# Kernel optimization log

Measured on AMD Instinct MI355X. Metric: run time of the kernel, lower is better.

The kernel has to match this reference:

```python
import jax, jax.numpy as jnp
import numpy as np

DT = 0.02
B = 524288
HID = 128


def setup_inputs() -> dict:
    key = jax.random.key(0)
    ks = jax.random.split(key, 11)
    def lin_init(k, fan_in, fan_out):
        # torch nn.Linear default: U(-1/sqrt(fan_in), 1/sqrt(fan_in))
        bound = 1.0 / np.sqrt(fan_in)
        kw, kb = jax.random.split(k)
        W = jax.random.uniform(kw, (fan_in, fan_out), jnp.float32, -bound, bound)
        b = jax.random.uniform(kb, (fan_out,), jnp.float32, -bound, bound)
        return W, b
    W1, b1 = lin_init(ks[0], 2, HID)
    W2, b2 = lin_init(ks[1], HID, HID)
    W3, b3 = lin_init(ks[2], HID, HID)
    W4, b4 = lin_init(ks[3], HID, 1)
    return {
        "q": jax.random.normal(ks[4], (B, 1), jnp.float32),
        "p": jax.random.normal(ks[5], (B, 1), jnp.float32),
        "F_ext": jax.random.normal(ks[6], (B, 1), jnp.float32),
        "W1": W1, "b1": b1, "W2": W2, "b2": b2,
        "W3": W3, "b3": b3, "W4": W4, "b4": b4,
    }


def reference(q, p, F_ext, W1, b1, W2, b2, W3, b3, W4, b4):
    def H_sum(q, p):
        s = jnp.concatenate([q, p], axis=1)          # [B, 2]
        h = jnp.tanh(s @ W1 + b1)                    # [B, 128]
        h = jnp.tanh(h @ W2 + b2)
        h = jnp.tanh(h @ W3 + b3)
        return jnp.sum(h @ W4 + b4)                  # scalar; samples independent
    dH_dq, dH_dp = jax.grad(H_sum, argnums=(0, 1))(q, p)
    dq_dt = dH_dp
    dp_dt = -dH_dq + F_ext
    return jnp.concatenate([dq_dt * DT, dp_dt * DT], axis=1)  # [B, 2]
```

## Files before the change

kernel.cpp:

```cpp
#include <hip/hip_runtime.h>

#define DT 0.02f

typedef __attribute__((ext_vector_type(8))) __bf16 bf16x8;
typedef __attribute__((ext_vector_type(4))) __bf16 bf16x4;
typedef __attribute__((ext_vector_type(4))) float  f32x4;

__device__ __forceinline__ float fast_tanh(float x){
    float e = __builtin_amdgcn_exp2f(x * 2.8853900817779268f);
    return 1.0f - 2.0f * __builtin_amdgcn_rcpf(e + 1.0f);
}
__device__ __forceinline__ char* ldsx(char* base, int m, int j){
    return base + (((m << 8) + (j << 1)) ^ ((m & 7) << 4));
}

template<int MODE>
__device__ __forceinline__ void hnn_gemm(const __bf16* __restrict__ Wg,
                                         char* Xbuf, char* Obuf,
                                         const float* __restrict__ bias,
                                         const float* __restrict__ w4,
                                         const bf16x4 (*m1)[4],
                                         int w, int l)
{
    const int lr = l & 15, lg = l >> 4;
    const int rbase = w * 32;

    f32x4 acc[2][4];
    #pragma unroll
    for (int mt = 0; mt < 2; ++mt)
        #pragma unroll
        for (int nt = 0; nt < 4; ++nt) acc[mt][nt] = 0.0f;

    #pragma unroll
    for (int ks = 0; ks < 4; ++ks){
        const int kb = ks * 32 + lg * 8;
        bf16x8 a[2], b[4];
        #pragma unroll
        for (int mt = 0; mt < 2; ++mt)
            a[mt] = *(const bf16x8*)(Wg + ((rbase + mt * 16 + lr) << 7) + kb);
        #pragma unroll
        for (int nt = 0; nt < 4; ++nt)
            b[nt] = *(const bf16x8*)ldsx(Xbuf, nt * 16 + lr, kb);
        #pragma unroll
        for (int mt = 0; mt < 2; ++mt)
            #pragma unroll
            for (int nt = 0; nt < 4; ++nt)
                acc[mt][nt] = __builtin_amdgcn_mfma_f32_16x16x32_bf16(
                    a[mt], b[nt], acc[mt][nt], 0, 0, 0);
    }

    if (MODE == 1){
        #pragma unroll
        for (int mt = 0; mt < 2; ++mt){
            const int j0 = rbase + mt * 16 + lg * 4;
            const f32x4 bv = *(const f32x4*)(bias + j0);
            #pragma unroll
            for (int nt = 0; nt < 4; ++nt){
                const int m = nt * 16 + lr;
                bf16x4 hv;
                #pragma unroll
                for (int jr = 0; jr < 4; ++jr)
                    hv[jr] = (__bf16)fast_tanh(acc[mt][nt][jr] + bv[jr]);
                *(bf16x4*)ldsx(Obuf, m, j0) = hv;
            }
        }
    } else if (MODE == 4){
        #pragma unroll
        for (int mt = 0; mt < 2; ++mt){
            const int j0 = rbase + mt * 16 + lg * 4;
            const f32x4 bv = *(const f32x4*)(bias + j0);
            const f32x4 wv = *(const f32x4*)(w4 + j0);
            #pragma unroll
            for (int nt = 0; nt < 4; ++nt){
                const int m = nt * 16 + lr;
                bf16x4 gv;
                #pragma unroll
                for (int jr = 0; jr < 4; ++jr){
                    float tt = fast_tanh(acc[mt][nt][jr] + bv[jr]);
                    gv[jr] = (__bf16)(wv[jr] * (1.0f - tt * tt));
                }
                *(bf16x4*)ldsx(Obuf, m, j0) = gv;
            }
        }
    } else if (MODE == 0){
        #pragma unroll
        for (int mt = 0; mt < 2; ++mt){
            const int j0 = rbase + mt * 16 + lg * 4;
            #pragma unroll
            for (int nt = 0; nt < 4; ++nt){
                const int m = nt * 16 + lr;
                bf16x4* hp = (bf16x4*)ldsx(Obuf, m, j0);
                bf16x4 hv = *hp, gv;
                #pragma unroll
                for (int jr = 0; jr < 4; ++jr){
                    float h = (float)hv[jr];
                    gv[jr] = (__bf16)(acc[mt][nt][jr] * (1.0f - h * h));
                }
                *hp = gv;
            }
        }
    } else {
        #pragma unroll
        for (int mt = 0; mt < 2; ++mt){
            const int j0 = rbase + mt * 16 + lg * 4;
            #pragma unroll
            for (int nt = 0; nt < 4; ++nt){
                const int m = nt * 16 + lr;
                const bf16x4 mv = m1[mt][nt];
                bf16x4 gv;
                #pragma unroll
                for (int jr = 0; jr < 4; ++jr)
                    gv[jr] = (__bf16)(acc[mt][nt][jr] * (float)mv[jr]);
                *(bf16x4*)ldsx(Obuf, m, j0) = gv;
            }
        }
    }
}

__global__ void hnn_prep(const float* __restrict__ W2, const float* __restrict__ W3,
                         __bf16* __restrict__ ws)
{
    int idx = blockIdx.x * 256 + threadIdx.x;
    int k = idx >> 7, n = idx & 127;
    __bf16 v2 = (__bf16)W2[idx];
    __bf16 v3 = (__bf16)W3[idx];
    ws[n * 128 + k]         = v2;
    ws[16384 + n * 128 + k] = v3;
    ws[32768 + idx]         = v2;
    ws[49152 + idx]         = v3;
}

__global__ __launch_bounds__(256, 4)
void hnn_main(const float* __restrict__ q, const float* __restrict__ p,
              const float* __restrict__ Fx,
              const float* __restrict__ W1, const float* __restrict__ b1,
              const float* __restrict__ b2, const float* __restrict__ b3,
              const float* __restrict__ W4,
              const __bf16* __restrict__ ws,
              float* __restrict__ out)
{
    __shared__ char bufA[16384];
    __shared__ char bufB[16384];
    const int t = threadIdx.x;
    const int w = t >> 6, l = t & 63;
    const int lr = l & 15, lg = l >> 4;
    const long mg0 = (long)blockIdx.x * 64;

    bf16x4 mask1[2][4];
    {
        const int rbase = w * 32;
        float qq[4], pp[4];
        #pragma unroll
        for (int nt = 0; nt < 4; ++nt){
            qq[nt] = q[mg0 + nt * 16 + lr];
            pp[nt] = p[mg0 + nt * 16 + lr];
        }
        #pragma unroll
        for (int mt = 0; mt < 2; ++mt){
            const int j0 = rbase + mt * 16 + lg * 4;
            const f32x4 wq = *(const f32x4*)(W1 + j0);
            const f32x4 wp = *(const f32x4*)(W1 + 128 + j0);
            const f32x4 bb = *(const f32x4*)(b1 + j0);
            #pragma unroll
            for (int nt = 0; nt < 4; ++nt){
                bf16x4 hv, mv;
                #pragma unroll
                for (int jr = 0; jr < 4; ++jr){
                    float h = fast_tanh(fmaf(qq[nt], wq[jr], fmaf(pp[nt], wp[jr], bb[jr])));
                    hv[jr] = (__bf16)h;
                    mv[jr] = (__bf16)(1.0f - h * h);
                }
                *(bf16x4*)ldsx(bufA, nt * 16 + lr, j0) = hv;
                mask1[mt][nt] = mv;
            }
        }
    }
    __syncthreads();
    hnn_gemm<1>(ws,         bufA, bufB, b2, nullptr, nullptr, w, l);
    __syncthreads();
    hnn_gemm<4>(ws + 16384, bufB, bufA, b3, W4, nullptr, w, l);
    __syncthreads();
    hnn_gemm<0>(ws + 49152, bufA, bufB, nullptr, nullptr, nullptr, w, l);
    __syncthreads();
    hnn_gemm<5>(ws + 32768, bufB, bufA, nullptr, nullptr, mask1, w, l);
    __syncthreads();

    {
        const int m = t & 63, q4 = t >> 6;
        float sdq = 0.f, sdp = 0.f;
        #pragma unroll
        for (int i = 0; i < 4; ++i){
            int j0 = q4 * 32 + i * 8;
            bf16x8 gv = *(const bf16x8*)ldsx(bufA, m, j0);
            f32x4 wq0 = *(const f32x4*)(W1 + j0),       wq1 = *(const f32x4*)(W1 + j0 + 4);
            f32x4 wp0 = *(const f32x4*)(W1 + 128 + j0), wp1 = *(const f32x4*)(W1 + 128 + j0 + 4);
            #pragma unroll
            for (int u = 0; u < 4; ++u){
                float g0 = (float)gv[u], g1v = (float)gv[4 + u];
                sdq = fmaf(g0, wq0[u], fmaf(g1v, wq1[u], sdq));
                sdp = fmaf(g0, wp0[u], fmaf(g1v, wp1[u], sdp));
            }
        }
        float2* red = (float2*)bufB;
        red[m * 4 + q4] = make_float2(sdq, sdp);
    }
    __syncthreads();
    if (t < 64){
        const float2* red = (const float2*)bufB;
        float2 r0 = red[t * 4 + 0], r1 = red[t * 4 + 1];
        float2 r2 = red[t * 4 + 2], r3 = red[t * 4 + 3];
        float dq = r0.x + r1.x + r2.x + r3.x;
        float dp = r0.y + r1.y + r2.y + r3.y;
        long gm = mg0 + t;
        float2 o;
        o.x = DT * dp;
        o.y = DT * (-dq + Fx[gm]);
        *(float2*)(out + gm * 2) = o;
    }
}

extern "C" void kernel_launch(void* const* d_in, const int* in_sizes, int n_in,
                              void* d_out, int out_size, void* d_ws, size_t ws_size,
                              hipStream_t stream) {
    const float* q   = (const float*)d_in[0];
    const float* p   = (const float*)d_in[1];
    const float* Fx  = (const float*)d_in[2];
    const float* W1  = (const float*)d_in[3];
    const float* b1  = (const float*)d_in[4];
    const float* W2  = (const float*)d_in[5];
    const float* b2  = (const float*)d_in[6];
    const float* W3  = (const float*)d_in[7];
    const float* b3  = (const float*)d_in[8];
    const float* W4  = (const float*)d_in[9];
    __bf16* ws = (__bf16*)d_ws;
    float* out = (float*)d_out;

    (void)in_sizes; (void)n_in; (void)out_size; (void)ws_size;

    hnn_prep<<<64, 256, 0, stream>>>(W2, W3, ws);
    hnn_main<<<8192, 256, 0, stream>>>(q, p, Fx, W1, b1, b2, b3, W4, ws, out);
}
```

Baseline: 234.1 us.

## Use 512-thread blocks of 128 samples with register-resident weight fragments prefetched

Each block now handles 128 samples with 8 waves. Each wave owns 16 output features across all 128 samples, so its A fragments (16 rows x 128 k) fit in registers. The next layer's weight fragment is prefetched into registers right after the current MFMA loop, overlapping global weight loads with the epilogue and barrier. LDS use doubles to 64 KB per block, which may limit occupancy. Each wave also does more LDS B-fragment reads per MFMA (8 B loads per A fragment).

```diff
diff --git a/kernel.cpp b/kernel.cpp
--- a/kernel.cpp
+++ b/kernel.cpp
@@ -14,105 +14,88 @@
     return base + (((m << 8) + (j << 1)) ^ ((m & 7) << 4));
 }
 
-template<int MODE>
-__device__ __forceinline__ void hnn_gemm(const __bf16* __restrict__ Wg,
+__device__ __forceinline__ void ld_afrag(const __bf16* __restrict__ Wg, int w, int l,
+                                         bf16x8 a[4]){
+    const int lr = l & 15, lg = l >> 4;
+    const __bf16* row = Wg + ((w * 16 + lr) << 7) + lg * 8;
+    #pragma unroll
+    for (int ks = 0; ks < 4; ++ks) a[ks] = *(const bf16x8*)(row + ks * 32);
+}
+
+template<int MODE, bool PRE>
+__device__ __forceinline__ void hnn_gemm(const bf16x8 a[4],
+                                         const __bf16* __restrict__ Wnext, bf16x8 anext[4],
                                          char* Xbuf, char* Obuf,
                                          const float* __restrict__ bias,
                                          const float* __restrict__ w4,
-                                         const bf16x4 (*m1)[4],
+                                         const bf16x4* m1,
                                          int w, int l)
 {
     const int lr = l & 15, lg = l >> 4;
-    const int rbase = w * 32;
-
-    f32x4 acc[2][4];
+    const int j0 = w * 16 + lg * 4;
+
+    f32x4 acc[8];
     #pragma unroll
-    for (int mt = 0; mt < 2; ++mt)
-        #pragma unroll
-        for (int nt = 0; nt < 4; ++nt) acc[mt][nt] = 0.0f;
+    for (int nt = 0; nt < 8; ++nt) acc[nt] = 0.0f;
 
     #pragma unroll
     for (int ks = 0; ks < 4; ++ks){
         const int kb = ks * 32 + lg * 8;
-        bf16x8 a[2], b[4];
-        #pragma unroll
-        for (int mt = 0; mt < 2; ++mt)
-            a[mt] = *(const bf16x8*)(Wg + ((rbase + mt * 16 + lr) << 7) + kb);
-        #pragma unroll
-        for (int nt = 0; nt < 4; ++nt)
+        bf16x8 b[8];
+        #pragma unroll
+        for (int nt = 0; nt < 8; ++nt)
             b[nt] = *(const bf16x8*)ldsx(Xbuf, nt * 16 + lr, kb);
         #pragma unroll
-        for (int mt = 0; mt < 2; ++mt)
-            #pragma unroll
-            for (int nt = 0; nt < 4; ++nt)
-                acc[mt][nt] = __builtin_amdgcn_mfma_f32_16x16x32_bf16(
-                    a[mt], b[nt], acc[mt][nt], 0, 0, 0);
-    }
+        for (int nt = 0; nt < 8; ++nt)
+            acc[nt] = __builtin_amdgcn_mfma_f32_16x16x32_bf16(a[ks], b[nt], acc[nt], 0, 0, 0);
+    }
+
+    if (PRE) ld_afrag(Wnext, w, l, anext);
 
     if (MODE == 1){
-        #pragma unroll
-        for (int mt = 0; mt < 2; ++mt){
-            const int j0 = rbase + mt * 16 + lg * 4;
-            const f32x4 bv = *(const f32x4*)(bias + j0);
-            #pragma unroll
-            for (int nt = 0; nt < 4; ++nt){
-                const int m = nt * 16 + lr;
-                bf16x4 hv;
-                #pragma unroll
-                for (int jr = 0; jr < 4; ++jr)
-                    hv[jr] = (__bf16)fast_tanh(acc[mt][nt][jr] + bv[jr]);
-                *(bf16x4*)ldsx(Obuf, m, j0) = hv;
-            }
+        const f32x4 bv = *(const f32x4*)(bias + j0);
+        #pragma unroll
+        for (int nt = 0; nt < 8; ++nt){
+            bf16x4 hv;
+            #pragma unroll
+            for (int jr = 0; jr < 4; ++jr)
+                hv[jr] = (__bf16)fast_tanh(acc[nt][jr] + bv[jr]);
+            *(bf16x4*)ldsx(Obuf, nt * 16 + lr, j0) = hv;
         }
     } else if (MODE == 4){
-        #pragma unroll
-        for (int mt = 0; mt < 2; ++mt){
-            const int j0 = rbase + mt * 16 + lg * 4;
-            const f32x4 bv = *(const f32x4*)(bias + j0);
-            const f32x4 wv = *(const f32x4*)(w4 + j0);
-            #pragma unroll
-            for (int nt = 0; nt < 4; ++nt){
-                const int m = nt * 16 + lr;
-                bf16x4 gv;
-                #pragma unroll
-                for (int jr = 0; jr < 4; ++jr){
-                    float tt = fast_tanh(acc[mt][nt][jr] + bv[jr]);
-                    gv[jr] = (__bf16)(wv[jr] * (1.0f - tt * tt));
-                }
-                *(bf16x4*)ldsx(Obuf, m, j0) = gv;
-            }
+        const f32x4 bv = *(const f32x4*)(bias + j0);
+        const f32x4 wv = *(const f32x4*)(w4 + j0);
+        #pragma unroll
+        for (int nt = 0; nt < 8; ++nt){
+            bf16x4 gv;
+            #pragma unroll
+            for (int jr = 0; jr < 4; ++jr){
+                float tt = fast_tanh(acc[nt][jr] + bv[jr]);
+                gv[jr] = (__bf16)(wv[jr] * (1.0f - tt * tt));
+            }
+            *(bf16x4*)ldsx(Obuf, nt * 16 + lr, j0) = gv;
         }
     } else if (MODE == 0){
         #pragma unroll
-        for (int mt = 0; mt < 2; ++mt){
-            const int j0 = rbase + mt * 16 + lg * 4;
-            #pragma unroll
-            for (int nt = 0; nt < 4; ++nt){
-                const int m = nt * 16 + lr;
-                bf16x4* hp = (bf16x4*)ldsx(Obuf, m, j0);
-                bf16x4 hv = *hp, gv;
-                #pragma unroll
-                for (int jr = 0; jr < 4; ++jr){
-                    float h = (float)hv[jr];
-                    gv[jr] = (__bf16)(acc[mt][nt][jr] * (1.0f - h * h));
-                }
-                *hp = gv;
-            }
+        for (int nt = 0; nt < 8; ++nt){
+            bf16x4* hp = (bf16x4*)ldsx(Obuf, nt * 16 + lr, j0);
+            bf16x4 hv = *hp, gv;
+            #pragma unroll
+            for (int jr = 0; jr < 4; ++jr){
+                float h = (float)hv[jr];
+                gv[jr] = (__bf16)(acc[nt][jr] * (1.0f - h * h));
+            }
+            *hp = gv;
         }
     } else {
         #pragma unroll
-        for (int mt = 0; mt < 2; ++mt){
-            const int j0 = rbase + mt * 16 + lg * 4;
-            #pragma unroll
-            for (int nt = 0; nt < 4; ++nt){
-                const int m = nt * 16 + lr;
-                const bf16x4 mv = m1[mt][nt];
-                bf16x4 gv;
-                #pragma unroll
-                for (int jr = 0; jr < 4; ++jr)
-                    gv[jr] = (__bf16)(acc[mt][nt][jr] * (float)mv[jr]);
-                *(bf16x4*)ldsx(Obuf, m, j0) = gv;
-            }
+        for (int nt = 0; nt < 8; ++nt){
+            const bf16x4 mv = m1[nt];
+            bf16x4 gv;
+            #pragma unroll
+            for (int jr = 0; jr < 4; ++jr)
+                gv[jr] = (__bf16)(acc[nt][jr] * (float)mv[jr]);
+            *(bf16x4*)ldsx(Obuf, nt * 16 + lr, j0) = gv;
         }
     }
 }
@@ -130,7 +113,7 @@
     ws[49152 + idx]         = v3;
 }
 
-__global__ __launch_bounds__(256, 4)
+__global__ __launch_bounds__(512, 4)
 void hnn_main(const float* __restrict__ q, const float* __restrict__ p,
               const float* __restrict__ Fx,
               const float* __restrict__ W1, const float* __restrict__ b1,
@@ -139,54 +122,48 @@
               const __bf16* __restrict__ ws,
               float* __restrict__ out)
 {
-    __shared__ char bufA[16384];
-    __shared__ char bufB[16384];
+    __shared__ char bufA[32768];
+    __shared__ char bufB[32768];
     const int t = threadIdx.x;
     const int w = t >> 6, l = t & 63;
     const int lr = l & 15, lg = l >> 4;
-    const long mg0 = (long)blockIdx.x * 64;
-
-    bf16x4 mask1[2][4];
+    const long mg0 = (long)blockIdx.x * 128;
+
+    bf16x4 mask1[8];
+    bf16x8 aF[4], aG[4];
     {
-        const int rbase = w * 32;
-        float qq[4], pp[4];
-        #pragma unroll
-        for (int nt = 0; nt < 4; ++nt){
-            qq[nt] = q[mg0 + nt * 16 + lr];
-            pp[nt] = p[mg0 + nt * 16 + lr];
-        }
-        #pragma unroll
-        for (int mt = 0; mt < 2; ++mt){
-            const int j0 = rbase + mt * 16 + lg * 4;
-            const f32x4 wq = *(const f32x4*)(W1 + j0);
-            const f32x4 wp = *(const f32x4*)(W1 + 128 + j0);
-            const f32x4 bb = *(const f32x4*)(b1 + j0);
-            #pragma unroll
-            for (int nt = 0; nt < 4; ++nt){
-                bf16x4 hv, mv;
-                #pragma unroll
-                for (int jr = 0; jr < 4; ++jr){
-                    float h = fast_tanh(fmaf(qq[nt], wq[jr], fmaf(pp[nt], wp[jr], bb[jr])));
-                    hv[jr] = (__bf16)h;
-                    mv[jr] = (__bf16)(1.0f - h * h);
-                }
-                *(bf16x4*)ldsx(bufA, nt * 16 + lr, j0) = hv;
-                mask1[mt][nt] = mv;
-            }
-        }
-    }
-    __syncthreads();
-    hnn_gemm<1>(ws,         bufA, bufB, b2, nullptr, nullptr, w, l);
-    __syncthreads();
-    hnn_gemm<4>(ws + 16384, bufB, bufA, b3, W4, nullptr, w, l);
-    __syncthreads();
-    hnn_gemm<0>(ws + 49152, bufA, bufB, nullptr, nullptr, nullptr, w, l);
-    __syncthreads();
-    hnn_gemm<5>(ws + 32768, bufB, bufA, nullptr, nullptr, mask1, w, l);
+        const int j0 = w * 16 + lg * 4;
+        const f32x4 wq = *(const f32x4*)(W1 + j0);
+        const f32x4 wp = *(const f32x4*)(W1 + 128 + j0);
+        const f32x4 bb = *(const f32x4*)(b1 + j0);
+        #pragma unroll
+        for (int nt = 0; nt < 8; ++nt){
+            const int m = nt * 16 + lr;
+            float qq = q[mg0 + m], pp = p[mg0 + m];
+            bf16x4 hv, mv;
+            #pragma unroll
+            for (int jr = 0; jr < 4; ++jr){
+                float h = fast_tanh(fmaf(qq, wq[jr], fmaf(pp, wp[jr], bb[jr])));
+                hv[jr] = (__bf16)h;
+                mv[jr] = (__bf16)(1.0f - h * h);
+            }
+            *(bf16x4*)ldsx(bufA, m, j0) = hv;
+            mask1[nt] = mv;
+        }
+    }
+    ld_afrag(ws, w, l, aF);
+    __syncthreads();
+    hnn_gemm<1, true >(aF, ws + 16384, aG, bufA, bufB, b2, nullptr, nullptr, w, l);
+    __syncthreads();
+    hnn_gemm<4, true >(aG, ws + 49152, aF, bufB, bufA, b3, W4, nullptr, w, l);
+    __syncthreads();
+    hnn_gemm<0, true >(aF, ws + 32768, aG, bufA, bufB, nullptr, nullptr, nullptr, w, l);
+    __syncthreads();
+    hnn_gemm<5, false>(aG, nullptr, aF, bufB, bufA, nullptr, nullptr, mask1, w, l);
     __syncthreads();
 
     {
-        const int m = t & 63, q4 = t >> 6;
+        const int m = t & 127, q4 = t >> 7;
         float sdq = 0.f, sdp = 0.f;
         #pragma unroll
         for (int i = 0; i < 4; ++i){
@@ -205,7 +182,7 @@
         red[m * 4 + q4] = make_float2(sdq, sdp);
     }
     __syncthreads();
-    if (t < 64){
+    if (t < 128){
         const float2* red = (const float2*)bufB;
         float2 r0 = red[t * 4 + 0], r1 = red[t * 4 + 1];
         float2 r2 = red[t * 4 + 2], r3 = red[t * 4 + 3];
@@ -238,5 +215,5 @@
     (void)in_sizes; (void)n_in; (void)out_size; (void)ws_size;
 
     hnn_prep<<<64, 256, 0, stream>>>(W2, W3, ws);
-    hnn_main<<<8192, 256, 0, stream>>>(q, p, Fx, W1, b1, b2, b3, W4, ws, out);
-}
+    hnn_main<<<4096, 512, 0, stream>>>(q, p, Fx, W1, b1, b2, b3, W4, ws, out);
+}
```

New measurement: 199.0 us. 15.0% less time.
